# Optimization experiments

Hardware: AMD Instinct MI355X
Metric: run time of the kernel (lower is better)

## Reference

```python
import jax, jax.numpy as jnp
import numpy as np

TEMPERATURE = 8.0  # sqrt(head_dim=64)
NEG_INF = -1e9


def setup_inputs() -> dict:
    key = jax.random.key(0)
    kq, kk, kv, km = jax.random.split(key, 4)
    B, H, S, D = 2, 16, 2048, 64
    q = jax.random.normal(kq, (B, H, S, D), dtype=jnp.float32)
    k = jax.random.normal(kk, (B, H, S, D), dtype=jnp.float32)
    v = jax.random.normal(kv, (B, H, S, D), dtype=jnp.float32)
    mask = jax.random.randint(km, (B, 1, 1, S), 0, 2, dtype=jnp.int32)
    return {"q": q, "k": k, "v": v, "mask": mask}


def reference(q, k, v, mask):
    # attn = (q / T) @ k^T  -> [B,H,S,S]
    scores = jnp.einsum("bhqd,bhkd->bhqk", q / TEMPERATURE, k)
    scores = jnp.where(mask == 0, NEG_INF, scores)
    attn = jax.nn.softmax(scores, axis=-1)  # dropout is identity in eval mode
    output = jnp.einsum("bhqk,bhkd->bhqd", attn, v)
    return (output, attn)
```

## Files before the change

### kernel.cpp

```cpp
#include <hip/hip_runtime.h>
#include <stdint.h>

constexpr int S   = 2048;
constexpr int D   = 64;
constexpr int BH  = 32;
constexpr int QT  = 64;
constexpr int KT  = 64;
constexpr int NTL = S / KT;
constexpr int LDP = 72;

using short8  = __attribute__((ext_vector_type(8))) short;
using float4v = __attribute__((ext_vector_type(4))) float;

static __device__ __forceinline__ unsigned short f2bf(float f) {
    union { float f; unsigned u; } x; x.f = f;
    unsigned u = x.u;
    u += 0x7fffu + ((u >> 16) & 1u);
    return (unsigned short)(u >> 16);
}

static __device__ __forceinline__ unsigned cvt_pk_bf16(float lo, float hi) {
    unsigned r;
    asm("v_cvt_pk_bf16_f32 %0, %1, %2" : "=v"(r) : "v"(lo), "v"(hi));
    return r;
}

static __device__ __forceinline__ void ld16(const unsigned short* g, unsigned short* ldsbase) {
    __builtin_amdgcn_global_load_lds(
        (const __attribute__((address_space(1))) void*)g,
        (__attribute__((address_space(3))) void*)ldsbase, 16, 0, 0);
}

__global__ __launch_bounds__(256) void pack_kernel(const float* __restrict__ k,
                                                   const float* __restrict__ v,
                                                   unsigned short* __restrict__ ws) {
    __shared__ __align__(16) unsigned short sT[64][LDP];
    const int blk = blockIdx.x;
    const int bh  = blk >> 5;
    const int k0  = (blk & 31) << 6;
    const int t   = threadIdx.x;
    unsigned short* dst = ws + (size_t)blk * 8192;

    const float* kp = k + ((size_t)bh * S + k0) * D;
#pragma unroll
    for (int i = 0; i < 4; ++i) {
        const int f4 = t + 256 * i;
        float4v val = ((const float4v*)kp)[f4];
        const int e = f4 * 4;
        const int r = e >> 6;
        const int c = e & 63;
        ushort4 pk;
        pk.x = f2bf(val.x); pk.y = f2bf(val.y); pk.z = f2bf(val.z); pk.w = f2bf(val.w);
        const int idx = r * 64 + (((c >> 3) ^ (r & 7)) << 3) + (c & 7);
        *(ushort4*)&dst[idx] = pk;
    }
    const float* vp = v + ((size_t)bh * S + k0) * D;
#pragma unroll
    for (int i = 0; i < 4; ++i) {
        const int f4 = t + 256 * i;
        float4v val = ((const float4v*)vp)[f4];
        const int e = f4 * 4;
        const int r = e >> 6;
        const int c = e & 63;
        sT[c + 0][r] = f2bf(val.x);
        sT[c + 1][r] = f2bf(val.y);
        sT[c + 2][r] = f2bf(val.z);
        sT[c + 3][r] = f2bf(val.w);
    }
    __syncthreads();
#pragma unroll
    for (int i = 0; i < 2; ++i) {
        const int f    = t + 256 * i;
        const int drow = f >> 3;
        const int ch   = f & 7;
        short8 val = *(const short8*)&sT[drow][ch * 8];
        const int idx = 4096 + drow * 64 + ((ch ^ (drow & 7)) << 3);
        *(short8*)&dst[idx] = val;
    }
}

__global__ __launch_bounds__(256, 4) void attn_kernel(const float* __restrict__ q,
                                                      const unsigned short* __restrict__ ws,
                                                      const int* __restrict__ mask,
                                                      float* __restrict__ out) {
    __shared__ __align__(16) unsigned short lbuf[2][8192];
    __shared__ float smF[S];

    const int tid  = threadIdx.x;
    const int wave = tid >> 6;
    const int lane = tid & 63;
    const int quad = lane >> 4;
    const int n16  = lane & 15;

    const int bx0 = blockIdx.x;
    const int bx  = (bx0 & 7) * 128 + (bx0 >> 3);
    const int bh  = bx >> 5;
    const int qt  = bx & 31;
    const int q0  = qt * QT;
    const int b   = bh >> 4;

    const float* qp = q + ((size_t)bh * S + q0) * D;
    const unsigned short* wsp = ws + (size_t)bh * NTL * 8192;

    {
        const int4* mp4 = (const int4*)(mask + b * S);
#pragma unroll
        for (int i = 0; i < 2; ++i) {
            const int f = tid + 256 * i;
            int4 m = mp4[f];
            const int e = f * 4;
            smF[e + 0] = m.x ? 1.f : 0.f;
            smF[e + 1] = m.y ? 1.f : 0.f;
            smF[e + 2] = m.z ? 1.f : 0.f;
            smF[e + 3] = m.w ? 1.f : 0.f;
        }
    }

    short8 aq0, aq1;
    {
        const float4v* qrow = (const float4v*)(qp + (size_t)(wave * 16 + n16) * D);
        float4v a = qrow[quad * 2], bq = qrow[quad * 2 + 1];
        float4v c = qrow[8 + quad * 2], d = qrow[8 + quad * 2 + 1];
        union { short8 s8; unsigned short u[8]; } t0, t1;
        t0.u[0] = f2bf(a.x * 0.125f);  t0.u[1] = f2bf(a.y * 0.125f);
        t0.u[2] = f2bf(a.z * 0.125f);  t0.u[3] = f2bf(a.w * 0.125f);
        t0.u[4] = f2bf(bq.x * 0.125f); t0.u[5] = f2bf(bq.y * 0.125f);
        t0.u[6] = f2bf(bq.z * 0.125f); t0.u[7] = f2bf(bq.w * 0.125f);
        t1.u[0] = f2bf(c.x * 0.125f);  t1.u[1] = f2bf(c.y * 0.125f);
        t1.u[2] = f2bf(c.z * 0.125f);  t1.u[3] = f2bf(c.w * 0.125f);
        t1.u[4] = f2bf(d.x * 0.125f);  t1.u[5] = f2bf(d.y * 0.125f);
        t1.u[6] = f2bf(d.z * 0.125f);  t1.u[7] = f2bf(d.w * 0.125f);
        aq0 = t0.s8; aq1 = t1.s8;
    }

    auto stage16 = [&](int bi, int tile) {
        const unsigned short* src = wsp + (size_t)tile * 8192;
        unsigned short* dstb = &lbuf[bi][0];
#pragma unroll
        for (int j = 0; j < 4; ++j) {
            const int ch = wave * 4 + j;
            ld16(src + ch * 512 + lane * 8, dstb + ch * 512);
        }
    };
    auto stage8 = [&](int bi, int tile) {
        const unsigned short* src = wsp + (size_t)tile * 8192;
        unsigned short* dstb = &lbuf[bi][0];
#pragma unroll
        for (int j = 0; j < 2; ++j) {
            const int ch = wave * 2 + j;
            ld16(src + ch * 512 + lane * 8, dstb + ch * 512);
        }
    };

    int koff[2][4], voff[2][4];
#pragma unroll
    for (int c = 0; c < 2; ++c)
#pragma unroll
        for (int nc = 0; nc < 4; ++nc) {
            koff[c][nc] = (nc * 16 + n16) * 64 + (((c * 4 + quad) ^ (n16 & 7)) << 3);
            voff[c][nc] = 4096 + (nc * 16 + n16) * 64 + (((c * 4 + quad) ^ (n16 & 7)) << 3);
        }

    float4v accO[4];
    const float4v zero4 = {0.f, 0.f, 0.f, 0.f};
#pragma unroll
    for (int nv = 0; nv < 4; ++nv) accO[nv] = zero4;
    float lsum = 0.f;

    stage16(0, 0);
    asm volatile("s_waitcnt lgkmcnt(0)" ::: "memory");
    for (int t = 0; t < NTL; ++t) {
        if (t < NTL - 1) {
            stage16((t + 1) & 1, t + 1);
            asm volatile("s_waitcnt vmcnt(4)" ::: "memory");
        } else {
            asm volatile("s_waitcnt vmcnt(0)" ::: "memory");
        }
        __builtin_amdgcn_sched_barrier(0);
        __builtin_amdgcn_s_barrier();

        const unsigned short* kb = &lbuf[t & 1][0];
        const int k0 = t * KT;

        short8 kf[8];
#pragma unroll
        for (int c = 0; c < 2; ++c)
#pragma unroll
            for (int nc = 0; nc < 4; ++nc)
                kf[c * 4 + nc] = *(const short8*)&kb[koff[c][nc]];
        float4v cf[4];
#pragma unroll
        for (int nc = 0; nc < 4; ++nc) cf[nc] = zero4;
        __builtin_amdgcn_s_setprio(1);
#pragma unroll
        for (int c = 0; c < 2; ++c) {
            const short8 aq = (c == 0) ? aq0 : aq1;
#pragma unroll
            for (int nc = 0; nc < 4; ++nc)
                cf[nc] = __builtin_amdgcn_mfma_f32_16x16x32_bf16(kf[c * 4 + nc], aq, cf[nc], 0, 0, 0);
        }
        __builtin_amdgcn_s_setprio(0);

        float p[4][4];
#pragma unroll
        for (int nc = 0; nc < 4; ++nc) {
            const float4v mf = *(const float4v*)&smF[k0 + nc * 16 + quad * 4];
            p[nc][0] = __expf(cf[nc][0]) * mf[0];
            p[nc][1] = __expf(cf[nc][1]) * mf[1];
            p[nc][2] = __expf(cf[nc][2]) * mf[2];
            p[nc][3] = __expf(cf[nc][3]) * mf[3];
        }
        {
            float s = 0.f;
#pragma unroll
            for (int nc = 0; nc < 4; ++nc)
#pragma unroll
                for (int r = 0; r < 4; ++r) s += p[nc][r];
            s += __shfl_xor(s, 16, 64);
            s += __shfl_xor(s, 32, 64);
            lsum += s;
        }

        unsigned w[8];
#pragma unroll
        for (int nc = 0; nc < 4; ++nc) {
            w[nc * 2 + 0] = cvt_pk_bf16(p[nc][0], p[nc][1]);
            w[nc * 2 + 1] = cvt_pk_bf16(p[nc][2], p[nc][3]);
        }
        unsigned X[4] = { w[0], w[1], w[4], w[5] };
        unsigned Y[4] = { w[2], w[3], w[6], w[7] };
        unsigned r1[4], r2[4];
#pragma unroll
        for (int dd = 0; dd < 4; ++dd) {
            const unsigned send1 = (quad & 2) ? X[dd] : Y[dd];
            r1[dd] = (unsigned)__shfl_xor((int)send1, 32, 64);
        }
#pragma unroll
        for (int dd = 0; dd < 4; ++dd) {
            const unsigned send2 = (quad == 1) ? X[dd] : (quad == 2) ? Y[dd] : r1[dd];
            r2[dd] = (unsigned)__shfl_xor((int)send2, 16, 64);
        }
        union { short8 s8; unsigned u[4]; } ap0, ap1;
        ap0.u[0] = (quad == 0) ? w[0] : (quad == 2) ? r1[0] : r2[0];
        ap0.u[1] = (quad == 0) ? w[1] : (quad == 2) ? r1[1] : r2[1];
        ap0.u[2] = (quad == 3) ? w[2] : (quad == 1) ? r1[0] : r2[0];
        ap0.u[3] = (quad == 3) ? w[3] : (quad == 1) ? r1[1] : r2[1];
        ap1.u[0] = (quad == 0) ? w[4] : (quad == 2) ? r1[2] : r2[2];
        ap1.u[1] = (quad == 0) ? w[5] : (quad == 2) ? r1[3] : r2[3];
        ap1.u[2] = (quad == 3) ? w[6] : (quad == 1) ? r1[2] : r2[2];
        ap1.u[3] = (quad == 3) ? w[7] : (quad == 1) ? r1[3] : r2[3];

        short8 vf[8];
#pragma unroll
        for (int kc = 0; kc < 2; ++kc)
#pragma unroll
            for (int nv = 0; nv < 4; ++nv)
                vf[kc * 4 + nv] = *(const short8*)&kb[voff[kc][nv]];
        __builtin_amdgcn_s_setprio(1);
#pragma unroll
        for (int kc = 0; kc < 2; ++kc) {
            const short8 ap = (kc == 0) ? ap0.s8 : ap1.s8;
#pragma unroll
            for (int nv = 0; nv < 4; ++nv)
                accO[nv] = __builtin_amdgcn_mfma_f32_16x16x32_bf16(ap, vf[kc * 4 + nv], accO[nv], 0, 0, 0);
        }
        __builtin_amdgcn_s_setprio(0);

        __builtin_amdgcn_s_barrier();
    }

    const float linv_sw = 1.0f / lsum;
    float linv_c[4];
#pragma unroll
    for (int r = 0; r < 4; ++r)
        linv_c[r] = __shfl(linv_sw, quad * 4 + r, 64);

    {
        const size_t obase = ((size_t)bh * S + q0 + wave * 16) * D;
#pragma unroll
        for (int nv = 0; nv < 4; ++nv)
#pragma unroll
            for (int r = 0; r < 4; ++r)
                out[obase + (size_t)(quad * 4 + r) * D + nv * 16 + n16] = accO[nv][r] * linv_c[r];
    }

    float* attn = out + (size_t)BH * S * D;
    const size_t arow = (size_t)bh * S * S + (size_t)(q0 + wave * 16 + n16) * S;

    stage8(0, 0);
    for (int t = 0; t < NTL; ++t) {
        if (t < NTL - 1) {
            stage8((t + 1) & 1, t + 1);
            asm volatile("s_waitcnt vmcnt(2)" ::: "memory");
        } else {
            asm volatile("s_waitcnt vmcnt(0)" ::: "memory");
        }
        __builtin_amdgcn_sched_barrier(0);
        __builtin_amdgcn_s_barrier();

        const unsigned short* kb = &lbuf[t & 1][0];
        const int k0 = t * KT;

        short8 kf[8];
#pragma unroll
        for (int c = 0; c < 2; ++c)
#pragma unroll
            for (int nc = 0; nc < 4; ++nc)
                kf[c * 4 + nc] = *(const short8*)&kb[koff[c][nc]];
        float4v cf[4];
#pragma unroll
        for (int nc = 0; nc < 4; ++nc) cf[nc] = zero4;
        __builtin_amdgcn_s_setprio(1);
#pragma unroll
        for (int c = 0; c < 2; ++c) {
            const short8 aq = (c == 0) ? aq0 : aq1;
#pragma unroll
            for (int nc = 0; nc < 4; ++nc)
                cf[nc] = __builtin_amdgcn_mfma_f32_16x16x32_bf16(kf[c * 4 + nc], aq, cf[nc], 0, 0, 0);
        }
        __builtin_amdgcn_s_setprio(0);
#pragma unroll
        for (int nc = 0; nc < 4; ++nc) {
            const float4v mf = *(const float4v*)&smF[k0 + nc * 16 + quad * 4];
            float4v wv;
            wv[0] = __expf(cf[nc][0]) * mf[0] * linv_sw;
            wv[1] = __expf(cf[nc][1]) * mf[1] * linv_sw;
            wv[2] = __expf(cf[nc][2]) * mf[2] * linv_sw;
            wv[3] = __expf(cf[nc][3]) * mf[3] * linv_sw;
            *(float4v*)&attn[arow + k0 + nc * 16 + quad * 4] = wv;
        }
        __builtin_amdgcn_s_barrier();
    }
}

extern "C" void kernel_launch(void* const* d_in, const int* in_sizes, int n_in,
                              void* d_out, int out_size, void* d_ws, size_t ws_size,
                              hipStream_t stream) {
    const float* q    = (const float*)d_in[0];
    const float* k    = (const float*)d_in[1];
    const float* v    = (const float*)d_in[2];
    const int*   mask = (const int*)d_in[3];
    unsigned short* ws = (unsigned short*)d_ws;
    float* out = (float*)d_out;

    pack_kernel<<<dim3(BH * NTL), dim3(256), 0, stream>>>(k, v, ws);
    attn_kernel<<<dim3(BH * (S / QT)), dim3(256), 0, stream>>>(q, ws, mask, out);
}
```

Before: 672.0 us.

## Double query tile to 128 rows with 512-thread blocks and triple-buffered K/V staging

Doubles the query tile per block (eight waves instead of four), so each staged K/V tile in LDS feeds twice as many query rows and the per-wave share of global-to-LDS copies is halved. The K/V staging moves from a double buffer to a three-deep ring with a prefetch distance of two tiles, and the vmcnt waits are adjusted to match. This cuts redundant K/V reads from L2 and hides more load latency, at the cost of more LDS per block (three 16 KB buffers), half as many blocks, and possibly lower occupancy.

```diff
diff --git a/kernel.cpp b/kernel.cpp
--- a/kernel.cpp
+++ b/kernel.cpp
@@ -4,7 +4,7 @@
 constexpr int S   = 2048;
 constexpr int D   = 64;
 constexpr int BH  = 32;
-constexpr int QT  = 64;
+constexpr int QT  = 128;
 constexpr int KT  = 64;
 constexpr int NTL = S / KT;
 constexpr int LDP = 72;
@@ -79,11 +79,11 @@
     }
 }
 
-__global__ __launch_bounds__(256, 4) void attn_kernel(const float* __restrict__ q,
+__global__ __launch_bounds__(512, 4) void attn_kernel(const float* __restrict__ q,
                                                       const unsigned short* __restrict__ ws,
                                                       const int* __restrict__ mask,
                                                       float* __restrict__ out) {
-    __shared__ __align__(16) unsigned short lbuf[2][8192];
+    __shared__ __align__(16) unsigned short lbuf[3][8192];
     __shared__ float smF[S];
 
     const int tid  = threadIdx.x;
@@ -93,9 +93,9 @@
     const int n16  = lane & 15;
 
     const int bx0 = blockIdx.x;
-    const int bx  = (bx0 & 7) * 128 + (bx0 >> 3);
-    const int bh  = bx >> 5;
-    const int qt  = bx & 31;
+    const int bx  = (bx0 & 7) * 64 + (bx0 >> 3);
+    const int bh  = bx >> 4;
+    const int qt  = bx & 15;
     const int q0  = qt * QT;
     const int b   = bh >> 4;
 
@@ -104,16 +104,12 @@
 
     {
         const int4* mp4 = (const int4*)(mask + b * S);
-#pragma unroll
-        for (int i = 0; i < 2; ++i) {
-            const int f = tid + 256 * i;
-            int4 m = mp4[f];
-            const int e = f * 4;
-            smF[e + 0] = m.x ? 1.f : 0.f;
-            smF[e + 1] = m.y ? 1.f : 0.f;
-            smF[e + 2] = m.z ? 1.f : 0.f;
-            smF[e + 3] = m.w ? 1.f : 0.f;
-        }
+        int4 m = mp4[tid];
+        const int e = tid * 4;
+        smF[e + 0] = m.x ? 1.f : 0.f;
+        smF[e + 1] = m.y ? 1.f : 0.f;
+        smF[e + 2] = m.z ? 1.f : 0.f;
+        smF[e + 3] = m.w ? 1.f : 0.f;
     }
 
     short8 aq0, aq1;
@@ -137,19 +133,16 @@
         const unsigned short* src = wsp + (size_t)tile * 8192;
         unsigned short* dstb = &lbuf[bi][0];
 #pragma unroll
-        for (int j = 0; j < 4; ++j) {
-            const int ch = wave * 4 + j;
+        for (int j = 0; j < 2; ++j) {
+            const int ch = wave * 2 + j;
             ld16(src + ch * 512 + lane * 8, dstb + ch * 512);
         }
     };
     auto stage8 = [&](int bi, int tile) {
         const unsigned short* src = wsp + (size_t)tile * 8192;
         unsigned short* dstb = &lbuf[bi][0];
-#pragma unroll
-        for (int j = 0; j < 2; ++j) {
-            const int ch = wave * 2 + j;
-            ld16(src + ch * 512 + lane * 8, dstb + ch * 512);
-        }
+        const int ch = wave;
+        ld16(src + ch * 512 + lane * 8, dstb + ch * 512);
     };
 
     int koff[2][4], voff[2][4];
@@ -168,18 +161,21 @@
     float lsum = 0.f;
 
     stage16(0, 0);
+    stage16(1, 1);
     asm volatile("s_waitcnt lgkmcnt(0)" ::: "memory");
     for (int t = 0; t < NTL; ++t) {
-        if (t < NTL - 1) {
-            stage16((t + 1) & 1, t + 1);
+        if (t + 2 < NTL) {
+            stage16((t + 2) % 3, t + 2);
             asm volatile("s_waitcnt vmcnt(4)" ::: "memory");
+        } else if (t + 1 < NTL) {
+            asm volatile("s_waitcnt vmcnt(2)" ::: "memory");
         } else {
             asm volatile("s_waitcnt vmcnt(0)" ::: "memory");
         }
         __builtin_amdgcn_sched_barrier(0);
         __builtin_amdgcn_s_barrier();
 
-        const unsigned short* kb = &lbuf[t & 1][0];
+        const unsigned short* kb = &lbuf[t % 3][0];
         const int k0 = t * KT;
 
         short8 kf[8];
@@ -288,17 +284,20 @@
     const size_t arow = (size_t)bh * S * S + (size_t)(q0 + wave * 16 + n16) * S;
 
     stage8(0, 0);
+    stage8(1, 1);
     for (int t = 0; t < NTL; ++t) {
-        if (t < NTL - 1) {
-            stage8((t + 1) & 1, t + 1);
+        if (t + 2 < NTL) {
+            stage8((t + 2) % 3, t + 2);
             asm volatile("s_waitcnt vmcnt(2)" ::: "memory");
+        } else if (t + 1 < NTL) {
+            asm volatile("s_waitcnt vmcnt(1)" ::: "memory");
         } else {
             asm volatile("s_waitcnt vmcnt(0)" ::: "memory");
         }
         __builtin_amdgcn_sched_barrier(0);
         __builtin_amdgcn_s_barrier();
 
-        const unsigned short* kb = &lbuf[t & 1][0];
+        const unsigned short* kb = &lbuf[t % 3][0];
         const int k0 = t * KT;
 
         short8 kf[8];
@@ -344,5 +343,5 @@
     float* out = (float*)d_out;
 
     pack_kernel<<<dim3(BH * NTL), dim3(256), 0, stream>>>(k, v, ws);
-    attn_kernel<<<dim3(BH * (S / QT)), dim3(256), 0, stream>>>(q, ws, mask, out);
-}
+    attn_kernel<<<dim3(BH * (S / QT)), dim3(512), 0, stream>>>(q, ws, mask, out);
+}
```

New measurement: 668.0 us. No clear change (-0.6%).
